# Kernel tuning notes

Hardware: AMD Instinct MI355X
Metric: run time of the kernel (lower is better)

## Reference

```python
import jax, jax.numpy as jnp
import numpy as np

# Module config: RoDAlignMax(aligned_height=9, aligned_width=9, spatial_scale=0.25)
# Internally RoDAlignFunction is called with aligned_height+1, aligned_width+1,
# then max_pool2d(kernel=2, stride=1) shrinks each spatial dim by 1.
AH, AW = 10, 10          # pre-pool sampling grid (aligned_{h,w} + 1)
SPATIAL_SCALE = 0.25


def _rod_align(features, rois, ah, aw, scale):
    """RoDAlign: uniform bilinear sampling grid over the WHOLE feature map,
    with samples falling INSIDE the ROI zeroed out (region-of-discard).
    features: [B,C,H,W], rois: [R,5]=(batch_ind,x1,y1,x2,y2) -> [R,C,ah,aw]."""
    B, C, H, W = features.shape
    dt = features.dtype
    bidx = rois[:, 0].astype(jnp.int32)                              # [R]
    x1 = rois[:, 1] * scale
    y1 = rois[:, 2] * scale
    x2 = rois[:, 3] * scale
    y2 = rois[:, 4] * scale
    # uniform grid spanning the full feature map
    h = jnp.arange(ah, dtype=dt) * ((H - 1.0) / (ah - 1.0))          # [AH]
    w = jnp.arange(aw, dtype=dt) * ((W - 1.0) / (aw - 1.0))          # [AW]
    h0 = jnp.minimum(jnp.floor(h), H - 2).astype(jnp.int32)
    w0 = jnp.minimum(jnp.floor(w), W - 2).astype(jnp.int32)
    hr = (h - h0.astype(dt))[:, None, None]                          # [AH,1,1]
    wr = (w - w0.astype(dt))[None, :, None]                          # [1,AW,1]
    b = bidx[:, None, None]                                          # [R,1,1]
    hi0 = h0[None, :, None]; hi1 = hi0 + 1                           # [1,AH,1]
    wi0 = w0[None, None, :]; wi1 = wi0 + 1                           # [1,1,AW]
    # four corner gathers; advanced idx dims go first -> [R,AH,AW,C]
    ul = features[b, :, hi0, wi0]
    ur = features[b, :, hi0, wi1]
    dl = features[b, :, hi1, wi0]
    dr = features[b, :, hi1, wi1]
    out = (ul * (1 - hr) * (1 - wr) + ur * (1 - hr) * wr
           + dl * hr * (1 - wr) + dr * hr * wr)                      # [R,AH,AW,C]
    # zero samples inside the ROI (the kept crop region is discarded)
    in_h = (h[None, :] >= y1[:, None]) & (h[None, :] <= y2[:, None])  # [R,AH]
    in_w = (w[None, :] >= x1[:, None]) & (w[None, :] <= x2[:, None])  # [R,AW]
    inside = in_h[:, :, None] & in_w[:, None, :]                      # [R,AH,AW]
    out = jnp.where(inside[..., None], jnp.zeros((), dt), out)
    return jnp.transpose(out, (0, 3, 1, 2))                           # [R,C,AH,AW]


def _maxpool2x2_s1(x):
    # max_pool2d(kernel_size=2, stride=1) on [..., H, W]
    return jnp.maximum(jnp.maximum(x[..., :-1, :-1], x[..., :-1, 1:]),
                       jnp.maximum(x[..., 1:, :-1], x[..., 1:, 1:]))


def setup_inputs() -> dict:
    key = jax.random.key(0)
    k1, k2, k3, k4, k5 = jax.random.split(key, 5)
    B, C, H, W = 4, 256, 64, 64
    R = 2048
    img = H / SPATIAL_SCALE  # 256.0, input-image coordinate extent
    features = jax.random.normal(k1, (B, C, H, W), dtype=jnp.float32)
    bidx = jax.random.randint(k2, (R,), 0, B).astype(jnp.float32)
    x1 = jax.random.uniform(k3, (R,), dtype=jnp.float32) * (img * 0.5)
    y1 = jax.random.uniform(k4, (R,), dtype=jnp.float32) * (img * 0.5)
    wh = jax.random.uniform(k5, (R, 2), dtype=jnp.float32) * (img * 0.45) + img * 0.05
    x2 = jnp.minimum(x1 + wh[:, 0], img - 1.0)
    y2 = jnp.minimum(y1 + wh[:, 1], img - 1.0)
    rois = jnp.stack([bidx, x1, y1, x2, y2], axis=1)  # [R,5]
    return {"features": features, "rois": rois}


def reference(features, rois):
    x = _rod_align(features, rois, AH, AW, SPATIAL_SCALE)  # [R,C,10,10]
    return _maxpool2x2_s1(x)                               # [R,C,9,9]
```

## Files before the change

kernel.cpp:

```cpp
#include <hip/hip_runtime.h>


#define NC 256
#define NR 2048

__global__ __launch_bounds__(128) void rod_gather2(const float* __restrict__ F,
                                                   float* __restrict__ G2) {
    int bc = blockIdx.x;
    int t  = threadIdx.x;
    if (t < 100) {
        int i = (t * 205) >> 11;
        int j = t - 10 * i;
        G2[bc * 100 + t] = F[(bc << 12) + i * 448 + j * 7];
    }
}

__global__ __launch_bounds__(256, 4) void rod_main2(const float* __restrict__ G2,
                                                    const float* __restrict__ rois,
                                                    float* __restrict__ out) {
    const int tid = threadIdx.x;
    const int r   = blockIdx.x;

    const float x1 = rois[r * 5 + 1] * 0.25f;
    const float y1 = rois[r * 5 + 2] * 0.25f;
    const float x2 = rois[r * 5 + 3] * 0.25f;
    const float y2 = rois[r * 5 + 4] * 0.25f;
    const int   b  = (int)rois[r * 5 + 0];

    unsigned inhM = 0u, inwM = 0u;
    #pragma unroll
    for (int t = 0; t < 10; ++t) {
        float s = 7.0f * (float)t;
        if ((s >= y1) && (s <= y2)) inhM |= (1u << t);
        if ((s >= x1) && (s <= x2)) inwM |= (1u << t);
    }

    const float* Gb  = G2 + b * 25600;
    float*       dst = out + (size_t)r * 20736;

    int c = (tid * 405) >> 15;
    int q = tid - 81 * c;

    #pragma unroll 4
    for (int k = 0; k < 81; ++k) {
        int i = (q * 57) >> 9;
        int j = q - 9 * i;

        const float* gp = Gb + c * 100 + i * 10 + j;
        float v00 = gp[0];
        float v01 = gp[1];
        float v10 = gp[10];
        float v11 = gp[11];

        unsigned hb = inhM >> i;
        unsigned wb = inwM >> j;
        float a00 = ((hb        & wb       ) & 1u) ? 0.0f : v00;
        float a01 = ((hb        & (wb >> 1)) & 1u) ? 0.0f : v01;
        float a10 = (((hb >> 1) & wb       ) & 1u) ? 0.0f : v10;
        float a11 = (((hb >> 1) & (wb >> 1)) & 1u) ? 0.0f : v11;

        dst[tid + (k << 8)] = fmaxf(fmaxf(a00, a01), fmaxf(a10, a11));

        q += 13; c += 3;
        if (q >= 81) { q -= 81; c += 1; }
    }
}

extern "C" void kernel_launch(void* const* d_in, const int* in_sizes, int n_in,
                              void* d_out, int out_size, void* d_ws, size_t ws_size,
                              hipStream_t stream) {
    const float* F    = (const float*)d_in[0];
    const float* rois = (const float*)d_in[1];
    float*       out  = (float*)d_out;
    float*       G2   = (float*)d_ws;

    rod_gather2<<<dim3(1024), dim3(128), 0, stream>>>(F, G2);
    rod_main2<<<dim3(NR), dim3(256), 0, stream>>>(G2, rois, out);
}
```

Baseline: 195.0 us.

## Assign one channel per thread with padded rows and register sliding-window maxpool

The gathered grid is padded to 12-float rows so each row can be read with aligned float4 loads. The main kernel now gives each thread one channel and walks the rows, keeping the previous masked row in registers so every sample is loaded once rather than four times. The cost is per-thread output stores at a stride of 81 floats, which are uncoalesced across the wave and rely on caches to merge writes. Register pressure also rises.

```diff
diff --git a/kernel.cpp b/kernel.cpp
--- a/kernel.cpp
+++ b/kernel.cpp
@@ -1,25 +1,29 @@
 #include <hip/hip_runtime.h>
 
 
-#define NC 256
 #define NR 2048
 
-__global__ __launch_bounds__(128) void rod_gather2(const float* __restrict__ F,
-                                                   float* __restrict__ G2) {
+typedef float f4a4  __attribute__((ext_vector_type(4), aligned(4)));
+typedef float f4a16 __attribute__((ext_vector_type(4), aligned(16)));
+
+__global__ __launch_bounds__(128) void rod_gather3(const float* __restrict__ F,
+                                                   float* __restrict__ G) {
     int bc = blockIdx.x;
     int t  = threadIdx.x;
-    if (t < 100) {
-        int i = (t * 205) >> 11;
-        int j = t - 10 * i;
-        G2[bc * 100 + t] = F[(bc << 12) + i * 448 + j * 7];
+    if (t < 120) {
+        int i = (t * 43) >> 9;
+        int j = t - 12 * i;
+        float v = 0.0f;
+        if (j < 10) v = F[(bc << 12) + i * 448 + j * 7];
+        G[bc * 120 + t] = v;
     }
 }
 
-__global__ __launch_bounds__(256, 4) void rod_main2(const float* __restrict__ G2,
-                                                    const float* __restrict__ rois,
-                                                    float* __restrict__ out) {
-    const int tid = threadIdx.x;
-    const int r   = blockIdx.x;
+__global__ __launch_bounds__(256) void rod_main3(const float* __restrict__ G,
+                                                 const float* __restrict__ rois,
+                                                 float* __restrict__ out) {
+    const int c = threadIdx.x;
+    const int r = blockIdx.x;
 
     const float x1 = rois[r * 5 + 1] * 0.25f;
     const float y1 = rois[r * 5 + 2] * 0.25f;
@@ -27,42 +31,55 @@
     const float y2 = rois[r * 5 + 4] * 0.25f;
     const int   b  = (int)rois[r * 5 + 0];
 
-    unsigned inhM = 0u, inwM = 0u;
+    unsigned inh = 0u, inw = 0u;
     #pragma unroll
     for (int t = 0; t < 10; ++t) {
         float s = 7.0f * (float)t;
-        if ((s >= y1) && (s <= y2)) inhM |= (1u << t);
-        if ((s >= x1) && (s <= x2)) inwM |= (1u << t);
+        if ((s >= y1) && (s <= y2)) inh |= (1u << t);
+        if ((s >= x1) && (s <= x2)) inw |= (1u << t);
     }
 
-    const float* Gb  = G2 + b * 25600;
-    float*       dst = out + (size_t)r * 20736;
+    const float* g   = G + (b * 256 + c) * 120;
+    float*       dst = out + (size_t)r * 20736 + c * 81;
 
-    int c = (tid * 405) >> 15;
-    int q = tid - 81 * c;
+    float m0[10];
+    {
+        f4a16 a = *(const f4a16*)(g);
+        f4a16 bq = *(const f4a16*)(g + 4);
+        float v8 = g[8], v9 = g[9];
+        unsigned wm = (inh & 1u) ? inw : 0u;
+        float v[10] = {a.x, a.y, a.z, a.w, bq.x, bq.y, bq.z, bq.w, v8, v9};
+        #pragma unroll
+        for (int j = 0; j < 10; ++j)
+            m0[j] = ((wm >> j) & 1u) ? 0.0f : v[j];
+    }
 
-    #pragma unroll 4
-    for (int k = 0; k < 81; ++k) {
-        int i = (q * 57) >> 9;
-        int j = q - 9 * i;
+    #pragma unroll
+    for (int i = 1; i < 10; ++i) {
+        const float* gr = g + i * 12;
+        f4a16 a  = *(const f4a16*)(gr);
+        f4a16 bq = *(const f4a16*)(gr + 4);
+        float v8 = gr[8], v9 = gr[9];
+        float v[10] = {a.x, a.y, a.z, a.w, bq.x, bq.y, bq.z, bq.w, v8, v9};
 
-        const float* gp = Gb + c * 100 + i * 10 + j;
-        float v00 = gp[0];
-        float v01 = gp[1];
-        float v10 = gp[10];
-        float v11 = gp[11];
+        unsigned wm = ((inh >> i) & 1u) ? inw : 0u;
+        float m1[10], t_[10];
+        #pragma unroll
+        for (int j = 0; j < 10; ++j) {
+            m1[j] = ((wm >> j) & 1u) ? 0.0f : v[j];
+            t_[j] = fmaxf(m0[j], m1[j]);
+        }
+        float o[9];
+        #pragma unroll
+        for (int j = 0; j < 9; ++j) o[j] = fmaxf(t_[j], t_[j + 1]);
 
-        unsigned hb = inhM >> i;
-        unsigned wb = inwM >> j;
-        float a00 = ((hb        & wb       ) & 1u) ? 0.0f : v00;
-        float a01 = ((hb        & (wb >> 1)) & 1u) ? 0.0f : v01;
-        float a10 = (((hb >> 1) & wb       ) & 1u) ? 0.0f : v10;
-        float a11 = (((hb >> 1) & (wb >> 1)) & 1u) ? 0.0f : v11;
+        float* dr = dst + (i - 1) * 9;
+        *(f4a4*)(dr)     = (f4a4){o[0], o[1], o[2], o[3]};
+        *(f4a4*)(dr + 4) = (f4a4){o[4], o[5], o[6], o[7]};
+        dr[8] = o[8];
 
-        dst[tid + (k << 8)] = fmaxf(fmaxf(a00, a01), fmaxf(a10, a11));
-
-        q += 13; c += 3;
-        if (q >= 81) { q -= 81; c += 1; }
+        #pragma unroll
+        for (int j = 0; j < 10; ++j) m0[j] = m1[j];
     }
 }
 
@@ -72,8 +89,8 @@
     const float* F    = (const float*)d_in[0];
     const float* rois = (const float*)d_in[1];
     float*       out  = (float*)d_out;
-    float*       G2   = (float*)d_ws;
+    float*       G    = (float*)d_ws;
 
-    rod_gather2<<<dim3(1024), dim3(128), 0, stream>>>(F, G2);
-    rod_main2<<<dim3(NR), dim3(256), 0, stream>>>(G2, rois, out);
+    rod_gather3<<<dim3(1024), dim3(128), 0, stream>>>(F, G);
+    rod_main3<<<dim3(NR), dim3(256), 0, stream>>>(G, rois, out);
 }
```

After: 243.6 us. +24.9%, slower.

## Precompute pairwise max table and rebuild masked 2x2 max from one vector load

Applied to the files above, without the earlier changes.

Replaces the sampled-grid gather with a table holding, for every pooling window, the row-pair and column-pair maxima of the four bilinear corner samples. The main kernel rebuilds the masked 2x2 max from a single 16-byte load plus the ROI bitmasks, instead of four scalar loads and four selects. Outputs are written with nontemporal stores to avoid polluting cache. The table is larger than the old gathered grid and relies on reasoning about which mask patterns can occur.

```diff
diff --git a/kernel.cpp b/kernel.cpp
--- a/kernel.cpp
+++ b/kernel.cpp
@@ -1,23 +1,32 @@
 #include <hip/hip_runtime.h>
 
 
-#define NC 256
 #define NR 2048
 
-__global__ __launch_bounds__(128) void rod_gather2(const float* __restrict__ F,
-                                                   float* __restrict__ G2) {
-    int bc = blockIdx.x;
-    int t  = threadIdx.x;
-    if (t < 100) {
-        int i = (t * 205) >> 11;
-        int j = t - 10 * i;
-        G2[bc * 100 + t] = F[(bc << 12) + i * 448 + j * 7];
+typedef float f4 __attribute__((ext_vector_type(4)));
+
+__global__ __launch_bounds__(256) void rod_table(const float* __restrict__ F,
+                                                 f4* __restrict__ T) {
+    int idx = blockIdx.x * 256 + threadIdx.x;
+    if (idx < 82944) {
+        unsigned bc = ((unsigned)idx * 25891u) >> 21;
+        int q = idx - 81 * (int)bc;
+        int i = (q * 57) >> 9;
+        int j = q - 9 * i;
+        const float* fp = F + ((int)bc << 12) + i * 448 + j * 7;
+        float v00 = fp[0], v01 = fp[7], v10 = fp[448], v11 = fp[455];
+        f4 t;
+        t.x = fmaxf(v00, v01);
+        t.y = fmaxf(v10, v11);
+        t.z = fmaxf(v00, v10);
+        t.w = fmaxf(v01, v11);
+        T[idx] = t;
     }
 }
 
-__global__ __launch_bounds__(256, 4) void rod_main2(const float* __restrict__ G2,
-                                                    const float* __restrict__ rois,
-                                                    float* __restrict__ out) {
+__global__ __launch_bounds__(256) void rod_main4(const f4* __restrict__ T,
+                                                 const float* __restrict__ rois,
+                                                 float* __restrict__ out) {
     const int tid = threadIdx.x;
     const int r   = blockIdx.x;
 
@@ -27,42 +36,39 @@
     const float y2 = rois[r * 5 + 4] * 0.25f;
     const int   b  = (int)rois[r * 5 + 0];
 
-    unsigned inhM = 0u, inwM = 0u;
+    unsigned inh = 0u, inw = 0u;
     #pragma unroll
     for (int t = 0; t < 10; ++t) {
         float s = 7.0f * (float)t;
-        if ((s >= y1) && (s <= y2)) inhM |= (1u << t);
-        if ((s >= x1) && (s <= x2)) inwM |= (1u << t);
+        if ((s >= y1) && (s <= y2)) inh |= (1u << t);
+        if ((s >= x1) && (s <= x2)) inw |= (1u << t);
     }
 
-    const float* Gb  = G2 + b * 25600;
-    float*       dst = out + (size_t)r * 20736;
+    const f4* Tb  = T + b * 20736;
+    float*    dst = out + (size_t)r * 20736;
 
-    int c = (tid * 405) >> 15;
-    int q = tid - 81 * c;
+    unsigned c0 = ((unsigned)tid * 25891u) >> 21;
+    int q  = tid - 81 * (int)c0;
+    int el = tid;
 
-    #pragma unroll 4
+    #pragma unroll 3
     for (int k = 0; k < 81; ++k) {
+        f4 t = Tb[el];
         int i = (q * 57) >> 9;
         int j = q - 9 * i;
+        unsigned hb = (inh >> i) & 3u;
+        unsigned wb = (inw >> j) & 3u;
 
-        const float* gp = Gb + c * 100 + i * 10 + j;
-        float v00 = gp[0];
-        float v01 = gp[1];
-        float v10 = gp[10];
-        float v11 = gp[11];
+        float rowA = (hb == 1u) ? t.y : ((hb == 2u) ? t.x : 0.0f);
+        float colA = (wb == 1u) ? t.w : ((wb == 2u) ? t.z : 0.0f);
+        float inMax  = fmaxf(fmaxf(rowA, colA), 0.0f);
+        float outMax = fmaxf(t.x, t.y);
+        bool  anyIn  = (hb != 0u) && (wb != 0u);
 
-        unsigned hb = inhM >> i;
-        unsigned wb = inwM >> j;
-        float a00 = ((hb        & wb       ) & 1u) ? 0.0f : v00;
-        float a01 = ((hb        & (wb >> 1)) & 1u) ? 0.0f : v01;
-        float a10 = (((hb >> 1) & wb       ) & 1u) ? 0.0f : v10;
-        float a11 = (((hb >> 1) & (wb >> 1)) & 1u) ? 0.0f : v11;
+        __builtin_nontemporal_store(anyIn ? inMax : outMax, dst + el);
 
-        dst[tid + (k << 8)] = fmaxf(fmaxf(a00, a01), fmaxf(a10, a11));
-
-        q += 13; c += 3;
-        if (q >= 81) { q -= 81; c += 1; }
+        el += 256;
+        q += 13; q = (q >= 81) ? q - 81 : q;
     }
 }
 
@@ -72,8 +78,8 @@
     const float* F    = (const float*)d_in[0];
     const float* rois = (const float*)d_in[1];
     float*       out  = (float*)d_out;
-    float*       G2   = (float*)d_ws;
+    f4*          T    = (f4*)d_ws;
 
-    rod_gather2<<<dim3(1024), dim3(128), 0, stream>>>(F, G2);
-    rod_main2<<<dim3(NR), dim3(256), 0, stream>>>(G2, rois, out);
+    rod_table<<<dim3(324), dim3(256), 0, stream>>>(F, T);
+    rod_main4<<<dim3(NR), dim3(256), 0, stream>>>(T, rois, out);
 }
```

Result: faster. 187.6 us (-3.8%).
